# Optimization experiments

Hardware: AMD Instinct MI355X
Metric: run time of the kernel (lower is better)

The kernel has to match this reference:

```python
import jax, jax.numpy as jnp
import numpy as np

N = 4096        # number_of_users
IN = 1000       # in_size (items)
H1, H2 = 2048, 1024
EMB = 512
HEADS = 8
OUT = 1000


def setup_inputs() -> dict:
    key = jax.random.key(0)
    ks = iter(jax.random.split(key, 32))
    def lin(i, o):
        return jax.random.normal(next(ks), (i, o), jnp.float32) * (1.0 / np.sqrt(i))
    inp = {"batch": jax.random.normal(next(ks), (N, IN), jnp.float32)}
    for p in ("q", "k", "v"):
        inp[p + "_w1"] = lin(IN, H1); inp[p + "_b1"] = jnp.zeros((H1,), jnp.float32)
        inp[p + "_w2"] = lin(H1, H2); inp[p + "_b2"] = jnp.zeros((H2,), jnp.float32)
        inp[p + "_w3"] = lin(H2, EMB); inp[p + "_b3"] = jnp.zeros((EMB,), jnp.float32)
    inp["wo_w"] = lin(EMB, OUT)
    inp["wo_b"] = jnp.zeros((OUT,), jnp.float32)
    return inp


def _mlp(x, w1, b1, w2, b2, w3, b3):
    h = jax.nn.relu(x @ w1 + b1)
    h = jax.nn.relu(h @ w2 + b2)
    return h @ w3 + b3


def _split_heads(x):
    # [N, EMB] -> [HEADS, N, depth]
    return x.reshape(N, HEADS, EMB // HEADS).transpose(1, 0, 2)


def reference(batch,
              q_w1, q_b1, q_w2, q_b2, q_w3, q_b3,
              k_w1, k_b1, k_w2, k_b2, k_w3, k_b3,
              v_w1, v_b1, v_w2, v_b2, v_w3, v_b3,
              wo_w, wo_b):
    q = _mlp(batch, q_w1, q_b1, q_w2, q_b2, q_w3, q_b3)
    k = _mlp(batch, k_w1, k_b1, k_w2, k_b2, k_w3, k_b3)
    v = _mlp(batch, v_w1, v_b1, v_w2, v_b2, v_w3, v_b3)
    qh = jax.nn.relu(_split_heads(q))
    kh = jax.nn.relu(_split_heads(k))
    vh = _split_heads(v)
    depth = EMB // HEADS
    # ReLU-normalized attention (no softmax): scores / row-sum
    scores = jnp.einsum('hnd,hmd->hnm', qh, kh) / jnp.sqrt(jnp.float32(depth))
    denom = jnp.sum(scores, axis=-1, keepdims=True) + 1e-8
    weights = scores / denom
    att = jnp.einsum('hnm,hmd->hnd', weights, vh)   # [H, N, depth]
    att = att.transpose(1, 0, 2).reshape(N, EMB)
    return att @ wo_w + wo_b
```

## Files before the change

kernel.cpp:

```cpp
#include <hip/hip_runtime.h>
#include <hip/hip_bf16.h>


typedef __attribute__((ext_vector_type(4))) float f32x4;
typedef __attribute__((ext_vector_type(4))) float float4v;
typedef __attribute__((ext_vector_type(8))) short bf16x8;

static constexpr size_t OFF_XB   = 0;
static constexpr size_t OFF_WT1  = OFF_XB   + 8388608;
static constexpr size_t OFF_WT2  = OFF_WT1  + 12582912;
static constexpr size_t OFF_WT3  = OFF_WT2  + 12582912;
static constexpr size_t OFF_MWT  = OFF_WT3  + 3145728;
static constexpr size_t OFF_B1C  = OFF_MWT  + 1048576;
static constexpr size_t OFF_H1   = OFF_B1C  + 24576;
static constexpr size_t OFF_H2   = OFF_H1   + 50331648;
static constexpr size_t OFF_QKV  = OFF_H2   + 25165824;
static constexpr size_t OFF_MP   = OFF_QKV  + 12582912;
static constexpr size_t OFF_MF   = OFF_MP   + 4259840;
static constexpr size_t OFF_QT   = OFF_MF   + 133120;

__device__ __forceinline__ void gload16(const __hip_bfloat16* g, __hip_bfloat16* l) {
  __builtin_amdgcn_global_load_lds(
      (const __attribute__((address_space(1))) void*)g,
      (__attribute__((address_space(3))) void*)l, 16, 0, 0);
}

__device__ __forceinline__ void xcd_rect(int idz, int gx, int cm, int cn,
                                         int& m, int& n) {
  const int xcd = idz & 7, slot = idz >> 3;
  const int nxr = gx / cn;
  const int xr = xcd % nxr, yr = xcd / nxr;
  m = yr * cm + (slot % cm);
  n = xr * cn + (slot / cm);
}

__global__ __launch_bounds__(256) void prep(
    const float* __restrict__ w1a, const float* __restrict__ w1b, const float* __restrict__ w1c,
    const float* __restrict__ w2a, const float* __restrict__ w2b, const float* __restrict__ w2c,
    const float* __restrict__ w3a, const float* __restrict__ w3b, const float* __restrict__ w3c,
    const float* __restrict__ batch,
    __hip_bfloat16* __restrict__ WT1, __hip_bfloat16* __restrict__ WT2,
    __hip_bfloat16* __restrict__ WT3, __hip_bfloat16* __restrict__ XB) {
  __shared__ float tile[32][33];
  const int b = blockIdx.x, t = threadIdx.x;
  if (b >= 13824) {
    int idx = (b - 13824) * 256 + t;
    int row = idx >> 8, c4 = (idx & 255) * 4;
    __hip_bfloat16 o[4];
    if (c4 < 1000) {
      float4v v = *reinterpret_cast<const float4v*>(&batch[(size_t)row * 1000 + c4]);
#pragma unroll
      for (int j = 0; j < 4; ++j) o[j] = __float2bfloat16(v[j]);
    } else {
#pragma unroll
      for (int j = 0; j < 4; ++j) o[j] = __float2bfloat16(0.f);
    }
    *reinterpret_cast<ushort4*>(&XB[(size_t)row * 1024 + c4]) =
        *reinterpret_cast<const ushort4*>(o);
    return;
  }
  const float* in; __hip_bfloat16* out; int K, N, Kpad, kb, nb;
  if (b < 6144) {
    int mat = b >> 11, r = b & 2047;
    const float* s[3] = {w1a, w1b, w1c};
    in = s[mat]; out = WT1 + (size_t)mat * 2048 * 1024;
    K = 1000; N = 2048; Kpad = 1024; kb = r & 31; nb = r >> 5;
  } else if (b < 12288) {
    int r = b - 6144; int mat = r >> 11; r &= 2047;
    const float* s[3] = {w2a, w2b, w2c};
    in = s[mat]; out = WT2 + (size_t)mat * 1024 * 2048;
    K = 2048; N = 1024; Kpad = 2048; kb = r & 63; nb = r >> 6;
  } else {
    int r = b - 12288; int mat = r >> 9; r &= 511;
    const float* s[3] = {w3a, w3b, w3c};
    in = s[mat]; out = WT3 + (size_t)mat * 512 * 1024;
    K = 1024; N = 512; Kpad = 1024; kb = r & 31; nb = r >> 5;
  }
  const int tx = t & 31, ty = t >> 5;
  const int kb32 = kb * 32, nb32 = nb * 32;
  for (int i = ty; i < 32; i += 8) {
    int k = kb32 + i, n = nb32 + tx;
    tile[i][tx] = (k < K && n < N) ? in[(size_t)k * N + n] : 0.f;
  }
  __syncthreads();
  for (int i = ty; i < 32; i += 8) {
    int n = nb32 + i, kp = kb32 + tx;
    out[(size_t)n * Kpad + kp] = __float2bfloat16(tile[tx][i]);
  }
}

__global__ __launch_bounds__(512, 2) void gemm_pp(
    const __hip_bfloat16* __restrict__ A, int lda, size_t Az,
    const __hip_bfloat16* __restrict__ B, int ldb, size_t Bz,
    const float* __restrict__ bias0, const float* __restrict__ bias1,
    const float* __restrict__ bias2,
    __hip_bfloat16* __restrict__ Cout, int ldc, size_t Cz,
    int NT, int mode, int cm, int cn) {
  __shared__ __hip_bfloat16 smA[2][8192];
  __shared__ __hip_bfloat16 smB[2][8192];
  const int t = threadIdx.x;
  const int z = blockIdx.z;
  int mt, nt;
  xcd_rect(blockIdx.y * gridDim.x + blockIdx.x, gridDim.x, cm, cn, mt, nt);
  const int m0 = mt * 256, n0 = nt * 256;
  A += (size_t)z * Az;
  B += (size_t)z * Bz;

  const int w = t >> 6, l = t & 63;
  const int wm = w >> 2, wn = w & 3;
  const int fr = l & 15, fq = l >> 4;

  const int r0 = t >> 2;
  const int cg = (t & 3) ^ ((t >> 3) & 3);
  const __hip_bfloat16* gA0 = A + (size_t)(m0 + r0) * lda + cg * 8;
  const __hip_bfloat16* gA1 = A + (size_t)(m0 + 128 + r0) * lda + cg * 8;
  const __hip_bfloat16* gB0 = B + (size_t)(n0 + r0) * ldb + cg * 8;
  const __hip_bfloat16* gB1 = B + (size_t)(n0 + 128 + r0) * ldb + cg * 8;

  const int soff = (fq ^ ((fr >> 1) & 3)) * 8;
  int offA[4], offB[2][2];
#pragma unroll
  for (int i = 0; i < 4; ++i) offA[i] = (wm * 64 + i * 16 + fr) * 32 + soff;
#pragma unroll
  for (int ng = 0; ng < 2; ++ng)
#pragma unroll
    for (int j = 0; j < 2; ++j)
      offB[ng][j] = (ng * 128 + wn * 32 + j * 16 + fr) * 32 + soff;

  f32x4 acc[8][4] = {};

  gload16(gA0, &smA[0][w * 512]);
  gload16(gA1, &smA[0][w * 512 + 4096]);
  gload16(gB0, &smB[0][w * 512]);
  gload16(gB1, &smB[0][w * 512 + 4096]);
  asm volatile("s_waitcnt vmcnt(0)" ::: "memory");
  __builtin_amdgcn_s_barrier();

  for (int T = 0; T < NT; ++T) {
    const int cur = T & 1, nxt = cur ^ 1;
    if (T > 0) {
      asm volatile("s_waitcnt vmcnt(0) lgkmcnt(0)" ::: "memory");
      __builtin_amdgcn_sched_barrier(0);
      __builtin_amdgcn_s_barrier();
    }
    bf16x8 af0[4], af1[4], bfv[2][2];
#pragma unroll
    for (int i = 0; i < 4; ++i) {
      af0[i] = *reinterpret_cast<const bf16x8*>(&smA[cur][offA[i]]);
      af1[i] = *reinterpret_cast<const bf16x8*>(&smA[cur][offA[i] + 4096]);
    }
#pragma unroll
    for (int ng = 0; ng < 2; ++ng)
#pragma unroll
      for (int j = 0; j < 2; ++j)
        bfv[ng][j] = *reinterpret_cast<const bf16x8*>(&smB[cur][offB[ng][j]]);
    if (T + 1 < NT) {
      const size_t ko = (size_t)(T + 1) * 32;
      gload16(gA0 + ko, &smA[nxt][w * 512]);
      gload16(gA1 + ko, &smA[nxt][w * 512 + 4096]);
      gload16(gB0 + ko, &smB[nxt][w * 512]);
      gload16(gB1 + ko, &smB[nxt][w * 512 + 4096]);
    }
    __builtin_amdgcn_s_setprio(1);
#pragma unroll
    for (int i = 0; i < 4; ++i)
#pragma unroll
      for (int ng = 0; ng < 2; ++ng)
#pragma unroll
        for (int j = 0; j < 2; ++j)
          acc[i][ng * 2 + j] = __builtin_amdgcn_mfma_f32_16x16x32_bf16(
              af0[i], bfv[ng][j], acc[i][ng * 2 + j], 0, 0, 0);
#pragma unroll
    for (int i = 0; i < 4; ++i)
#pragma unroll
      for (int ng = 0; ng < 2; ++ng)
#pragma unroll
        for (int j = 0; j < 2; ++j)
          acc[4 + i][ng * 2 + j] = __builtin_amdgcn_mfma_f32_16x16x32_bf16(
              af1[i], bfv[ng][j], acc[4 + i][ng * 2 + j], 0, 0, 0);
    __builtin_amdgcn_s_setprio(0);
  }

  __hip_bfloat16* C = Cout + (size_t)z * Cz;
  const float* bz = (z == 0) ? bias0 : ((z == 1) ? bias1 : bias2);
  float bvv[4];
#pragma unroll
  for (int nj = 0; nj < 4; ++nj) {
    const int col = n0 + (nj >> 1) * 128 + wn * 32 + (nj & 1) * 16 + fr;
    if (mode == 1) {
      const float* bsel = (col < 2048) ? bias0 : ((col < 4096) ? bias1 : bias2);
      bvv[nj] = bsel[col & 2047];
    } else {
      bvv[nj] = bz[col];
    }
  }
#pragma unroll
  for (int mi = 0; mi < 8; ++mi) {
    const int rowb = m0 + (mi >> 2) * 128 + wm * 64 + (mi & 3) * 16 + fq * 4;
#pragma unroll
    for (int nj = 0; nj < 4; ++nj) {
      const int col = n0 + (nj >> 1) * 128 + wn * 32 + (nj & 1) * 16 + fr;
#pragma unroll
      for (int rr = 0; rr < 4; ++rr) {
        float v = fmaxf(acc[mi][nj][rr] + bvv[nj], 0.f);
        C[(size_t)(rowb + rr) * ldc + col] = __float2bfloat16(v);
      }
    }
  }
}

__global__ __launch_bounds__(256) void gemm_bt(
    const __hip_bfloat16* __restrict__ A, int lda, size_t Az,
    const __hip_bfloat16* __restrict__ B, int ldb, size_t Bz,
    const float* __restrict__ bias0, const float* __restrict__ bias1,
    const float* __restrict__ bias2,
    void* __restrict__ Cout, int ldc, size_t Cz,
    int nlimit, int K, int epi, int cm, int cn) {
  __shared__ __hip_bfloat16 As[128 * 32];
  __shared__ __hip_bfloat16 Bs[128 * 32];
  const int t = threadIdx.x;
  const int z = blockIdx.z;
  int mt, nt;
  xcd_rect(blockIdx.y * gridDim.x + blockIdx.x, gridDim.x, cm, cn, mt, nt);
  const int m0 = mt * 128, n0 = nt * 128;
  A += (size_t)z * Az;
  B += (size_t)z * Bz;
  const float* bias = (z == 0) ? bias0 : ((z == 1) ? bias1 : bias2);
  const int w = t >> 6, l = t & 63;
  const int wm = (w >> 1) * 64, wn = (w & 1) * 64;
  const int fr = l & 15, fq = l >> 4;
  const int sr = t >> 2, sc = (t & 3) * 8;

  f32x4 acc[4][4] = {};

  const __hip_bfloat16* ga = A + (size_t)(m0 + sr) * lda + sc;
  const __hip_bfloat16* gb = B + (size_t)(n0 + sr) * ldb + sc;
  __hip_bfloat16* la = As + w * 512;
  __hip_bfloat16* lb = Bs + w * 512;

  for (int k0 = 0; k0 < K; k0 += 32) {
    gload16(ga, la);
    gload16(ga + (size_t)64 * lda, la + 2048);
    gload16(gb, lb);
    gload16(gb + (size_t)64 * ldb, lb + 2048);
    ga += 32; gb += 32;
    __syncthreads();
    bf16x8 af[4], bfr[4];
#pragma unroll
    for (int i = 0; i < 4; ++i) {
      af[i]  = *reinterpret_cast<const bf16x8*>(&As[(wm + i * 16 + fr) * 32 + fq * 8]);
      bfr[i] = *reinterpret_cast<const bf16x8*>(&Bs[(wn + i * 16 + fr) * 32 + fq * 8]);
    }
#pragma unroll
    for (int i = 0; i < 4; ++i)
#pragma unroll
      for (int j = 0; j < 4; ++j)
        acc[i][j] = __builtin_amdgcn_mfma_f32_16x16x32_bf16(af[i], bfr[j], acc[i][j], 0, 0, 0);
    __syncthreads();
  }

  const bool dorelu = (epi == 3 && z < 2);
  float bv[4];
#pragma unroll
  for (int j = 0; j < 4; ++j) {
    int col = n0 + wn + j * 16 + fr;
    bv[j] = (col < nlimit) ? bias[col] : 0.f;
  }
#pragma unroll
  for (int i = 0; i < 4; ++i) {
#pragma unroll
    for (int j = 0; j < 4; ++j) {
      int col = n0 + wn + j * 16 + fr;
#pragma unroll
      for (int r = 0; r < 4; ++r) {
        int row = m0 + wm + i * 16 + fq * 4 + r;
        float v = acc[i][j][r] + bv[j];
        if (dorelu) v = fmaxf(v, 0.f);
        if (epi == 2) {
          if (col < nlimit)
            ((float*)Cout)[(size_t)row * ldc + col] = v;
        } else {
          ((__hip_bfloat16*)Cout + (size_t)z * Cz)[(size_t)row * ldc + col] = __float2bfloat16(v);
        }
      }
    }
  }
}

__global__ __launch_bounds__(256) void kv_outer(const __hip_bfloat16* __restrict__ QKV, int ld,
                                                float* __restrict__ part) {
  __shared__ __hip_bfloat16 kt[128][64];
  __shared__ __hip_bfloat16 vt[128][64];
  const int t = threadIdx.x;
  const int n0 = blockIdx.x * 128;
  const int h = blockIdx.y;
#pragma unroll
  for (int it = 0; it < 4; ++it) {
    int r = it * 32 + (t >> 3);
    int c = (t & 7) * 8;
    const __hip_bfloat16* kr = &QKV[(size_t)(n0 + r) * ld + 512 + h * 64 + c];
    const __hip_bfloat16* vr = &QKV[(size_t)(n0 + r) * ld + 1024 + h * 64 + c];
    *reinterpret_cast<bf16x8*>(&kt[r][c]) = *reinterpret_cast<const bf16x8*>(kr);
    *reinterpret_cast<bf16x8*>(&vt[r][c]) = *reinterpret_cast<const bf16x8*>(vr);
  }
  __syncthreads();
  const int i = t >> 2, j0 = (t & 3) << 4;
  float acc[16] = {};
  float ks = 0.f;
  for (int r = 0; r < 128; ++r) {
    float kv = __bfloat162float(kt[r][i]);
    ks += kv;
    bf16x8 va = *reinterpret_cast<const bf16x8*>(&vt[r][j0]);
    bf16x8 vb = *reinterpret_cast<const bf16x8*>(&vt[r][j0 + 8]);
#pragma unroll
    for (int jj = 0; jj < 8; ++jj) {
      ushort ua = (ushort)((const short*)&va)[jj];
      ushort ub = (ushort)((const short*)&vb)[jj];
      acc[jj]     += kv * __bfloat162float(*(const __hip_bfloat16*)&ua);
      acc[8 + jj] += kv * __bfloat162float(*(const __hip_bfloat16*)&ub);
    }
  }
  float* dst = part + ((size_t)blockIdx.x * 8 + h) * 4160;
#pragma unroll
  for (int jj = 0; jj < 16; ++jj) dst[i * 64 + j0 + jj] = acc[jj];
  if ((t & 3) == 0) dst[4096 + i] = ks;
}

__global__ void reduce_m(const float* __restrict__ part, float* __restrict__ Mfin) {
  int h = blockIdx.x, t = threadIdx.x;
  for (int idx = t; idx < 4160; idx += 256) {
    float s = 0.f;
    for (int c = 0; c < 32; ++c) s += part[((size_t)c * 8 + h) * 4160 + idx];
    Mfin[(size_t)h * 4160 + idx] = s;
  }
}

__global__ __launch_bounds__(256) void mwq(const float* __restrict__ Mfin,
                                           const float* __restrict__ wo,
                                           __hip_bfloat16* __restrict__ MWT,
                                           const __hip_bfloat16* __restrict__ QKV,
                                           __hip_bfloat16* __restrict__ QT) {
  const int t = threadIdx.x;
  if (blockIdx.x < 32) {
    __shared__ float Ml[64][64];
    const int h = blockIdx.x >> 2;
    const int j = (blockIdx.x & 3) * 256 + t;
    const float* M = Mfin + (size_t)h * 4160;
    for (int e = t; e < 4096; e += 256)
      Ml[e >> 6][e & 63] = M[e];
    __syncthreads();
    float wcol[64];
    const bool valid = (j < 1000);
#pragma unroll
    for (int d = 0; d < 64; ++d)
      wcol[d] = valid ? wo[(size_t)(h * 64 + d) * 1000 + j] : 0.f;
    short ob[64];
#pragma unroll
    for (int i = 0; i < 64; ++i) {
      float a = 0.f;
#pragma unroll
      for (int d = 0; d < 64; ++d) a += Ml[i][d] * wcol[d];
      __hip_bfloat16 bb = __float2bfloat16(a);
      ob[i] = *(const short*)&bb;
    }
    __hip_bfloat16* dst = MWT + (size_t)j * 512 + h * 64;
#pragma unroll
    for (int v = 0; v < 8; ++v)
      *reinterpret_cast<bf16x8*>(dst + v * 8) = *reinterpret_cast<const bf16x8*>(&ob[v * 8]);
  } else {
    const int bid = blockIdx.x - 32;
    const int r = bid * 4 + (t >> 6);
    const int c = (t & 63) * 8;
    const int h = (t & 63) >> 3;
    bf16x8 qv = *reinterpret_cast<const bf16x8*>(&QKV[(size_t)r * 1536 + c]);
    float qf[8];
#pragma unroll
    for (int j = 0; j < 8; ++j) {
      ushort u = (ushort)((const short*)&qv)[j];
      qf[j] = __bfloat162float(*(const __hip_bfloat16*)&u);
    }
    const float* ks = Mfin + (size_t)h * 4160 + 4096 + (c & 63);
    float s = 0.f;
#pragma unroll
    for (int j = 0; j < 8; ++j) s += qf[j] * ks[j];
    s += __shfl_xor(s, 1, 8);
    s += __shfl_xor(s, 2, 8);
    s += __shfl_xor(s, 4, 8);
    const float inv = 0.125f / (s * 0.125f + 1e-8f);
    bf16x8 o;
#pragma unroll
    for (int j = 0; j < 8; ++j) {
      __hip_bfloat16 bb = __float2bfloat16(qf[j] * inv);
      ((short*)&o)[j] = *(const short*)&bb;
    }
    *reinterpret_cast<bf16x8*>(&QT[(size_t)r * 512 + c]) = o;
  }
}

extern "C" void kernel_launch(void* const* d_in, const int* in_sizes, int n_in,
                              void* d_out, int out_size, void* d_ws, size_t ws_size,
                              hipStream_t stream) {
  const float* batch = (const float*)d_in[0];
  const float* w1[3] = {(const float*)d_in[1],  (const float*)d_in[7],  (const float*)d_in[13]};
  const float* b1[3] = {(const float*)d_in[2],  (const float*)d_in[8],  (const float*)d_in[14]};
  const float* w2[3] = {(const float*)d_in[3],  (const float*)d_in[9],  (const float*)d_in[15]};
  const float* b2[3] = {(const float*)d_in[4],  (const float*)d_in[10], (const float*)d_in[16]};
  const float* w3[3] = {(const float*)d_in[5],  (const float*)d_in[11], (const float*)d_in[17]};
  const float* b3[3] = {(const float*)d_in[6],  (const float*)d_in[12], (const float*)d_in[18]};
  const float* wow   = (const float*)d_in[19];
  const float* wob   = (const float*)d_in[20];

  char* ws = (char*)d_ws;
  __hip_bfloat16* XB  = (__hip_bfloat16*)(ws + OFF_XB);
  __hip_bfloat16* WT1 = (__hip_bfloat16*)(ws + OFF_WT1);
  __hip_bfloat16* WT2 = (__hip_bfloat16*)(ws + OFF_WT2);
  __hip_bfloat16* WT3 = (__hip_bfloat16*)(ws + OFF_WT3);
  __hip_bfloat16* MWT = (__hip_bfloat16*)(ws + OFF_MWT);
  __hip_bfloat16* H1  = (__hip_bfloat16*)(ws + OFF_H1);
  __hip_bfloat16* H2  = (__hip_bfloat16*)(ws + OFF_H2);
  __hip_bfloat16* QKV = (__hip_bfloat16*)(ws + OFF_QKV);
  float*          MP  = (float*)(ws + OFF_MP);
  float*          MF  = (float*)(ws + OFF_MF);
  __hip_bfloat16* QT  = (__hip_bfloat16*)(ws + OFF_QT);
  float*          OUT = (float*)d_out;

  prep<<<17920, 256, 0, stream>>>(w1[0], w1[1], w1[2], w2[0], w2[1], w2[2],
                                  w3[0], w3[1], w3[2], batch, WT1, WT2, WT3, XB);

  gemm_pp<<<dim3(24, 16, 1), 512, 0, stream>>>(XB, 1024, 0, WT1, 1024, 0,
                                               b1[0], b1[1], b1[2], H1, 6144, 0,
                                               32, 1, 8, 6);
  gemm_pp<<<dim3(4, 16, 3), 512, 0, stream>>>(H1, 6144, 2048, WT2, 2048, (size_t)1024 * 2048,
                                              b2[0], b2[1], b2[2], H2, 3072, 1024,
                                              64, 0, 4, 2);
  gemm_bt<<<dim3(4, 32, 3), 256, 0, stream>>>(H2, 3072, 1024, WT3, 1024, (size_t)512 * 1024,
                                              b3[0], b3[1], b3[2], QKV, 1536, 512,
                                              512, 1024, 3, 8, 2);

  kv_outer<<<dim3(32, 8), 256, 0, stream>>>(QKV, 1536, MP);
  reduce_m<<<8, 256, 0, stream>>>(MP, MF);
  mwq<<<1056, 256, 0, stream>>>(MF, wow, MWT, QKV, QT);

  gemm_bt<<<dim3(8, 32, 1), 256, 0, stream>>>(QT, 512, 0, MWT, 512, 0,
                                              wob, wob, wob, OUT, 1000, 0,
                                              1000, 512, 2, 8, 4);

  (void)in_sizes; (void)n_in; (void)out_size; (void)ws_size;
}
```

Before: 295.7 us.

## Unify GEMMs into one 128x128 double-buffered kernel with XCD-aware 3D tile mapping

Replaces the 256x256 ping-pong GEMM (512 threads) and the single-buffered 128x128 gemm_bt with one 128x128, 256-thread kernel. The new kernel uses double-buffered async LDS loads, a swizzled LDS layout and a generalized XCD block mapping that includes the z dimension. All four GEMM launches now use it, with epilogue modes for relu/bias variants. The large MLP GEMMs lose the register-level reuse of the 256 tiles in exchange for more blocks and occupancy, while the small QKV and output GEMMs gain prefetch overlap.

```diff
diff --git a/kernel.cpp b/kernel.cpp
--- a/kernel.cpp
+++ b/kernel.cpp
@@ -25,13 +25,18 @@
       (__attribute__((address_space(3))) void*)l, 16, 0, 0);
 }
 
-__device__ __forceinline__ void xcd_rect(int idz, int gx, int cm, int cn,
-                                         int& m, int& n) {
-  const int xcd = idz & 7, slot = idz >> 3;
+__device__ __forceinline__ void xcd_map(int gx, int gy, int cm, int cn,
+                                        int& zz, int& mt, int& nt) {
+  const int gid = (blockIdx.z * gy + blockIdx.y) * gx + blockIdx.x;
+  const int xcd = gid & 7;
+  const int slot = gid >> 3;
+  const int per = cm * cn;
+  zz = slot / per;
+  const int rem = slot % per;
   const int nxr = gx / cn;
   const int xr = xcd % nxr, yr = xcd / nxr;
-  m = yr * cm + (slot % cm);
-  n = xr * cn + (slot / cm);
+  mt = yr * cm + rem % cm;
+  nt = xr * cn + rem / cm;
 }
 
 __global__ __launch_bounds__(256) void prep(
@@ -89,50 +94,47 @@
   }
 }
 
-__global__ __launch_bounds__(512, 2) void gemm_pp(
+__global__ __launch_bounds__(256) void gemm_fast(
     const __hip_bfloat16* __restrict__ A, int lda, size_t Az,
     const __hip_bfloat16* __restrict__ B, int ldb, size_t Bz,
     const float* __restrict__ bias0, const float* __restrict__ bias1,
     const float* __restrict__ bias2,
-    __hip_bfloat16* __restrict__ Cout, int ldc, size_t Cz,
-    int NT, int mode, int cm, int cn) {
-  __shared__ __hip_bfloat16 smA[2][8192];
-  __shared__ __hip_bfloat16 smB[2][8192];
+    void* __restrict__ Cout, int ldc, size_t Cz,
+    int nlimit, int NT, int epi, int cm, int cn) {
+  __shared__ __hip_bfloat16 smA[2][4096];
+  __shared__ __hip_bfloat16 smB[2][4096];
   const int t = threadIdx.x;
-  const int z = blockIdx.z;
-  int mt, nt;
-  xcd_rect(blockIdx.y * gridDim.x + blockIdx.x, gridDim.x, cm, cn, mt, nt);
-  const int m0 = mt * 256, n0 = nt * 256;
-  A += (size_t)z * Az;
-  B += (size_t)z * Bz;
+  int zz, mt, nt;
+  xcd_map(gridDim.x, gridDim.y, cm, cn, zz, mt, nt);
+  const int m0 = mt * 128, n0 = nt * 128;
+  A += (size_t)zz * Az;
+  B += (size_t)zz * Bz;
 
   const int w = t >> 6, l = t & 63;
-  const int wm = w >> 2, wn = w & 3;
+  const int wm = (w >> 1) * 64, wn = (w & 1) * 64;
   const int fr = l & 15, fq = l >> 4;
 
   const int r0 = t >> 2;
   const int cg = (t & 3) ^ ((t >> 3) & 3);
   const __hip_bfloat16* gA0 = A + (size_t)(m0 + r0) * lda + cg * 8;
-  const __hip_bfloat16* gA1 = A + (size_t)(m0 + 128 + r0) * lda + cg * 8;
+  const __hip_bfloat16* gA1 = gA0 + (size_t)64 * lda;
   const __hip_bfloat16* gB0 = B + (size_t)(n0 + r0) * ldb + cg * 8;
-  const __hip_bfloat16* gB1 = B + (size_t)(n0 + 128 + r0) * ldb + cg * 8;
+  const __hip_bfloat16* gB1 = gB0 + (size_t)64 * ldb;
 
   const int soff = (fq ^ ((fr >> 1) & 3)) * 8;
-  int offA[4], offB[2][2];
-#pragma unroll
-  for (int i = 0; i < 4; ++i) offA[i] = (wm * 64 + i * 16 + fr) * 32 + soff;
-#pragma unroll
-  for (int ng = 0; ng < 2; ++ng)
-#pragma unroll
-    for (int j = 0; j < 2; ++j)
-      offB[ng][j] = (ng * 128 + wn * 32 + j * 16 + fr) * 32 + soff;
-
-  f32x4 acc[8][4] = {};
+  int offA[4], offB[4];
+#pragma unroll
+  for (int i = 0; i < 4; ++i) {
+    offA[i] = (wm + i * 16 + fr) * 32 + soff;
+    offB[i] = (wn + i * 16 + fr) * 32 + soff;
+  }
+
+  f32x4 acc[4][4] = {};
 
   gload16(gA0, &smA[0][w * 512]);
-  gload16(gA1, &smA[0][w * 512 + 4096]);
+  gload16(gA1, &smA[0][w * 512 + 2048]);
   gload16(gB0, &smB[0][w * 512]);
-  gload16(gB1, &smB[0][w * 512 + 4096]);
+  gload16(gB1, &smB[0][w * 512 + 2048]);
   asm volatile("s_waitcnt vmcnt(0)" ::: "memory");
   __builtin_amdgcn_s_barrier();
 
@@ -143,144 +145,59 @@
       __builtin_amdgcn_sched_barrier(0);
       __builtin_amdgcn_s_barrier();
     }
-    bf16x8 af0[4], af1[4], bfv[2][2];
+    bf16x8 af[4], bf[4];
 #pragma unroll
     for (int i = 0; i < 4; ++i) {
-      af0[i] = *reinterpret_cast<const bf16x8*>(&smA[cur][offA[i]]);
-      af1[i] = *reinterpret_cast<const bf16x8*>(&smA[cur][offA[i] + 4096]);
-    }
-#pragma unroll
-    for (int ng = 0; ng < 2; ++ng)
-#pragma unroll
-      for (int j = 0; j < 2; ++j)
-        bfv[ng][j] = *reinterpret_cast<const bf16x8*>(&smB[cur][offB[ng][j]]);
+      af[i] = *reinterpret_cast<const bf16x8*>(&smA[cur][offA[i]]);
+      bf[i] = *reinterpret_cast<const bf16x8*>(&smB[cur][offB[i]]);
+    }
     if (T + 1 < NT) {
       const size_t ko = (size_t)(T + 1) * 32;
       gload16(gA0 + ko, &smA[nxt][w * 512]);
-      gload16(gA1 + ko, &smA[nxt][w * 512 + 4096]);
+      gload16(gA1 + ko, &smA[nxt][w * 512 + 2048]);
       gload16(gB0 + ko, &smB[nxt][w * 512]);
-      gload16(gB1 + ko, &smB[nxt][w * 512 + 4096]);
+      gload16(gB1 + ko, &smB[nxt][w * 512 + 2048]);
     }
     __builtin_amdgcn_s_setprio(1);
 #pragma unroll
     for (int i = 0; i < 4; ++i)
 #pragma unroll
-      for (int ng = 0; ng < 2; ++ng)
-#pragma unroll
-        for (int j = 0; j < 2; ++j)
-          acc[i][ng * 2 + j] = __builtin_amdgcn_mfma_f32_16x16x32_bf16(
-              af0[i], bfv[ng][j], acc[i][ng * 2 + j], 0, 0, 0);
-#pragma unroll
-    for (int i = 0; i < 4; ++i)
-#pragma unroll
-      for (int ng = 0; ng < 2; ++ng)
-#pragma unroll
-        for (int j = 0; j < 2; ++j)
-          acc[4 + i][ng * 2 + j] = __builtin_amdgcn_mfma_f32_16x16x32_bf16(
-              af1[i], bfv[ng][j], acc[4 + i][ng * 2 + j], 0, 0, 0);
+      for (int j = 0; j < 4; ++j)
+        acc[i][j] = __builtin_amdgcn_mfma_f32_16x16x32_bf16(af[i], bf[j], acc[i][j], 0, 0, 0);
     __builtin_amdgcn_s_setprio(0);
   }
 
-  __hip_bfloat16* C = Cout + (size_t)z * Cz;
-  const float* bz = (z == 0) ? bias0 : ((z == 1) ? bias1 : bias2);
-  float bvv[4];
-#pragma unroll
-  for (int nj = 0; nj < 4; ++nj) {
-    const int col = n0 + (nj >> 1) * 128 + wn * 32 + (nj & 1) * 16 + fr;
-    if (mode == 1) {
+  const float* bz = (zz == 0) ? bias0 : ((zz == 1) ? bias1 : bias2);
+  const bool dorelu = (epi == 1) || (epi == 4) || (epi == 3 && zz < 2);
+  float bv[4];
+#pragma unroll
+  for (int j = 0; j < 4; ++j) {
+    const int col = n0 + wn + j * 16 + fr;
+    if (epi == 4) {
       const float* bsel = (col < 2048) ? bias0 : ((col < 4096) ? bias1 : bias2);
-      bvv[nj] = bsel[col & 2047];
+      bv[j] = bsel[col & 2047];
+    } else if (epi == 2) {
+      bv[j] = (col < nlimit) ? bias0[col] : 0.f;
     } else {
-      bvv[nj] = bz[col];
-    }
-  }
-#pragma unroll
-  for (int mi = 0; mi < 8; ++mi) {
-    const int rowb = m0 + (mi >> 2) * 128 + wm * 64 + (mi & 3) * 16 + fq * 4;
-#pragma unroll
-    for (int nj = 0; nj < 4; ++nj) {
-      const int col = n0 + (nj >> 1) * 128 + wn * 32 + (nj & 1) * 16 + fr;
+      bv[j] = bz[col];
+    }
+  }
+#pragma unroll
+  for (int i = 0; i < 4; ++i) {
+#pragma unroll
+    for (int j = 0; j < 4; ++j) {
+      const int col = n0 + wn + j * 16 + fr;
 #pragma unroll
       for (int rr = 0; rr < 4; ++rr) {
-        float v = fmaxf(acc[mi][nj][rr] + bvv[nj], 0.f);
-        C[(size_t)(rowb + rr) * ldc + col] = __float2bfloat16(v);
-      }
-    }
-  }
-}
-
-__global__ __launch_bounds__(256) void gemm_bt(
-    const __hip_bfloat16* __restrict__ A, int lda, size_t Az,
-    const __hip_bfloat16* __restrict__ B, int ldb, size_t Bz,
-    const float* __restrict__ bias0, const float* __restrict__ bias1,
-    const float* __restrict__ bias2,
-    void* __restrict__ Cout, int ldc, size_t Cz,
-    int nlimit, int K, int epi, int cm, int cn) {
-  __shared__ __hip_bfloat16 As[128 * 32];
-  __shared__ __hip_bfloat16 Bs[128 * 32];
-  const int t = threadIdx.x;
-  const int z = blockIdx.z;
-  int mt, nt;
-  xcd_rect(blockIdx.y * gridDim.x + blockIdx.x, gridDim.x, cm, cn, mt, nt);
-  const int m0 = mt * 128, n0 = nt * 128;
-  A += (size_t)z * Az;
-  B += (size_t)z * Bz;
-  const float* bias = (z == 0) ? bias0 : ((z == 1) ? bias1 : bias2);
-  const int w = t >> 6, l = t & 63;
-  const int wm = (w >> 1) * 64, wn = (w & 1) * 64;
-  const int fr = l & 15, fq = l >> 4;
-  const int sr = t >> 2, sc = (t & 3) * 8;
-
-  f32x4 acc[4][4] = {};
-
-  const __hip_bfloat16* ga = A + (size_t)(m0 + sr) * lda + sc;
-  const __hip_bfloat16* gb = B + (size_t)(n0 + sr) * ldb + sc;
-  __hip_bfloat16* la = As + w * 512;
-  __hip_bfloat16* lb = Bs + w * 512;
-
-  for (int k0 = 0; k0 < K; k0 += 32) {
-    gload16(ga, la);
-    gload16(ga + (size_t)64 * lda, la + 2048);
-    gload16(gb, lb);
-    gload16(gb + (size_t)64 * ldb, lb + 2048);
-    ga += 32; gb += 32;
-    __syncthreads();
-    bf16x8 af[4], bfr[4];
-#pragma unroll
-    for (int i = 0; i < 4; ++i) {
-      af[i]  = *reinterpret_cast<const bf16x8*>(&As[(wm + i * 16 + fr) * 32 + fq * 8]);
-      bfr[i] = *reinterpret_cast<const bf16x8*>(&Bs[(wn + i * 16 + fr) * 32 + fq * 8]);
-    }
-#pragma unroll
-    for (int i = 0; i < 4; ++i)
-#pragma unroll
-      for (int j = 0; j < 4; ++j)
-        acc[i][j] = __builtin_amdgcn_mfma_f32_16x16x32_bf16(af[i], bfr[j], acc[i][j], 0, 0, 0);
-    __syncthreads();
-  }
-
-  const bool dorelu = (epi == 3 && z < 2);
-  float bv[4];
-#pragma unroll
-  for (int j = 0; j < 4; ++j) {
-    int col = n0 + wn + j * 16 + fr;
-    bv[j] = (col < nlimit) ? bias[col] : 0.f;
-  }
-#pragma unroll
-  for (int i = 0; i < 4; ++i) {
-#pragma unroll
-    for (int j = 0; j < 4; ++j) {
-      int col = n0 + wn + j * 16 + fr;
-#pragma unroll
-      for (int r = 0; r < 4; ++r) {
-        int row = m0 + wm + i * 16 + fq * 4 + r;
-        float v = acc[i][j][r] + bv[j];
+        const int row = m0 + wm + i * 16 + fq * 4 + rr;
+        float v = acc[i][j][rr] + bv[j];
         if (dorelu) v = fmaxf(v, 0.f);
         if (epi == 2) {
           if (col < nlimit)
             ((float*)Cout)[(size_t)row * ldc + col] = v;
         } else {
-          ((__hip_bfloat16*)Cout + (size_t)z * Cz)[(size_t)row * ldc + col] = __float2bfloat16(v);
+          ((__hip_bfloat16*)Cout + (size_t)zz * Cz)[(size_t)row * ldc + col] =
+              __float2bfloat16(v);
         }
       }
     }
@@ -427,23 +344,25 @@
   prep<<<17920, 256, 0, stream>>>(w1[0], w1[1], w1[2], w2[0], w2[1], w2[2],
                                   w3[0], w3[1], w3[2], batch, WT1, WT2, WT3, XB);
 
-  gemm_pp<<<dim3(24, 16, 1), 512, 0, stream>>>(XB, 1024, 0, WT1, 1024, 0,
-                                               b1[0], b1[1], b1[2], H1, 6144, 0,
-                                               32, 1, 8, 6);
-  gemm_pp<<<dim3(4, 16, 3), 512, 0, stream>>>(H1, 6144, 2048, WT2, 2048, (size_t)1024 * 2048,
-                                              b2[0], b2[1], b2[2], H2, 3072, 1024,
-                                              64, 0, 4, 2);
-  gemm_bt<<<dim3(4, 32, 3), 256, 0, stream>>>(H2, 3072, 1024, WT3, 1024, (size_t)512 * 1024,
-                                              b3[0], b3[1], b3[2], QKV, 1536, 512,
-                                              512, 1024, 3, 8, 2);
+  gemm_fast<<<dim3(48, 32, 1), 256, 0, stream>>>(XB, 1024, 0, WT1, 1024, 0,
+                                                 b1[0], b1[1], b1[2], H1, 6144, 0,
+                                                 6144, 32, 4, 16, 12);
+  gemm_fast<<<dim3(8, 32, 3), 256, 0, stream>>>(H1, 6144, 2048, WT2, 2048,
+                                                (size_t)1024 * 2048,
+                                                b2[0], b2[1], b2[2], H2, 3072, 1024,
+                                                1024, 64, 1, 8, 4);
+  gemm_fast<<<dim3(4, 32, 3), 256, 0, stream>>>(H2, 3072, 1024, WT3, 1024,
+                                                (size_t)512 * 1024,
+                                                b3[0], b3[1], b3[2], QKV, 1536, 512,
+                                                512, 32, 3, 8, 2);
 
   kv_outer<<<dim3(32, 8), 256, 0, stream>>>(QKV, 1536, MP);
   reduce_m<<<8, 256, 0, stream>>>(MP, MF);
   mwq<<<1056, 256, 0, stream>>>(MF, wow, MWT, QKV, QT);
 
-  gemm_bt<<<dim3(8, 32, 1), 256, 0, stream>>>(QT, 512, 0, MWT, 512, 0,
-                                              wob, wob, wob, OUT, 1000, 0,
-                                              1000, 512, 2, 8, 4);
+  gemm_fast<<<dim3(8, 32, 1), 256, 0, stream>>>(QT, 512, 0, MWT, 512, 0,
+                                                wob, wob, wob, OUT, 1000, 0,
+                                                1000, 16, 2, 8, 4);
 
   (void)in_sizes; (void)n_in; (void)out_size; (void)ws_size;
 }
```

New measurement: 282.3 us. -4.5%, faster.
